# Performance work log

Hardware: AMD Instinct MI355X
Metric: run time of the kernel (lower is better)

## Reference

```python
import jax, jax.numpy as jnp
import numpy as np
import math

B, L, D, K = 4, 2048, 1024, 3
PAD = K // 2
EPS_LN = 1e-5
EPS_NORM = 1e-12


def dwsep_conv(x_bld, dw, dwb, pw, pwb):
    # x_bld: [B, L, D] -> depthwise conv over L (groups=D) then pointwise 1x1
    x = jnp.transpose(x_bld, (0, 2, 1))  # [B, D, L]
    y = jax.lax.conv_general_dilated(
        x, dw, window_strides=(1,), padding=[(PAD, PAD)],
        feature_group_count=D, dimension_numbers=("NCH", "OIH", "NCH"))
    y = y + dwb[None, :, None]
    y = jnp.einsum("bcl,oc->bol", y, pw) + pwb[None, :, None]
    return jnp.transpose(y, (0, 2, 1))  # [B, L, D]


def l2norm(x):
    n = jnp.sqrt(jnp.sum(x * x, axis=-1, keepdims=True))
    return x / jnp.maximum(n, EPS_NORM)


def layernorm(x, g, b):
    mu = jnp.mean(x, axis=-1, keepdims=True)
    var = jnp.mean((x - mu) ** 2, axis=-1, keepdims=True)
    return (x - mu) * jax.lax.rsqrt(var + EPS_LN) * g + b


def setup_inputs() -> dict:
    key = jax.random.key(0)
    ks = jax.random.split(key, 24)
    s = 0.02
    def w(k, shape, scale=s):
        return (jax.random.normal(k, shape, dtype=jnp.float32) * scale)
    inp = {
        "x": jax.random.normal(ks[0], (B, L, D), dtype=jnp.float32),
        "wq": w(ks[1], (D, D)), "bq": jnp.zeros((D,), jnp.float32),
        "wk": w(ks[2], (D, D)), "bk": jnp.zeros((D,), jnp.float32),
        "wv": w(ks[3], (D, D)), "bv": jnp.zeros((D,), jnp.float32),
        "dwq": w(ks[4], (D, 1, K), 0.1), "dwq_b": jnp.zeros((D,), jnp.float32),
        "pwq": w(ks[5], (D, D)), "pwq_b": jnp.zeros((D,), jnp.float32),
        "dwk": w(ks[6], (D, 1, K), 0.1), "dwk_b": jnp.zeros((D,), jnp.float32),
        "pwk": w(ks[7], (D, D)), "pwk_b": jnp.zeros((D,), jnp.float32),
        "dwv": w(ks[8], (D, 1, K), 0.1), "dwv_b": jnp.zeros((D,), jnp.float32),
        "pwv": w(ks[9], (D, D)), "pwv_b": jnp.zeros((D,), jnp.float32),
        "wg": w(ks[10], (D, D)), "bg": jnp.zeros((D,), jnp.float32),
        "wo": w(ks[11], (D, D)), "bo": jnp.zeros((D,), jnp.float32),
        "mem_w": w(ks[12], (D, D)),
        "ln_g": jnp.ones((D,), jnp.float32),
        "ln_b": jnp.zeros((D,), jnp.float32),
    }
    return inp


def reference(x, wq, bq, wk, bk, wv, bv,
              dwq, dwq_b, pwq, pwq_b,
              dwk, dwk_b, pwk, pwk_b,
              dwv, dwv_b, pwv, pwv_b,
              wg, bg, wo, bo, mem_w, ln_g, ln_b):
    residual = x
    Q = jax.nn.silu(jnp.einsum("bld,ed->ble", x, wq) + bq)
    Kt = jax.nn.silu(jnp.einsum("bld,ed->ble", x, wk) + bk)
    V = jax.nn.silu(jnp.einsum("bld,ed->ble", x, wv) + bv)
    Q = dwsep_conv(Q, dwq, dwq_b, pwq, pwq_b)
    Kt = dwsep_conv(Kt, dwk, dwk_b, pwk, pwk_b)
    V = dwsep_conv(V, dwv, dwv_b, pwv, pwv_b)
    Qn = l2norm(Q)
    Kn = l2norm(Kt)
    scores = jnp.einsum("bqd,bkd->bqk", Qn, Kn) / math.sqrt(D)
    attn = jax.nn.softmax(scores, axis=-1)
    attn_out = jnp.einsum("bqk,bkd->bqd", attn, V)
    gate = jax.nn.sigmoid(jnp.einsum("bld,ed->ble", attn_out, wg) + bg)
    gated = gate * attn_out
    out = jnp.einsum("bld,ed->ble", gated, wo) + bo + residual
    out = layernorm(out, ln_g, ln_b)
    mem_pred = jnp.einsum("bld,de->ble", Kn, mem_w)
    mem_loss = jnp.mean((mem_pred - V) ** 2)
    return (out, mem_loss)
```

## Files before the change

### kernel.cpp

```cpp
#include <hip/hip_runtime.h>
#include <stdint.h>

typedef __attribute__((ext_vector_type(8))) short short8;
typedef __attribute__((ext_vector_type(4))) short short4v;
typedef __attribute__((ext_vector_type(4))) float f32x4;

#define DEV static __device__ __forceinline__

static constexpr int LL = 2048;
static constexpr int DD = 1024;
static constexpr long long BLD = 8388608LL;
static constexpr long long SLD = 2097152LL;
static constexpr long long SLLB = 4194304LL;

DEV short f2bf(float f) {
    uint32_t u = __builtin_bit_cast(uint32_t, f);
    u += 0x7fffu + ((u >> 16) & 1u);
    return (short)(u >> 16);
}
DEV float bf2f(short s) {
    uint32_t u = ((uint32_t)(uint16_t)s) << 16;
    return __builtin_bit_cast(float, u);
}

DEV float waveSum(float v) {
#pragma unroll
    for (int o = 32; o; o >>= 1) v += __shfl_down(v, o);
    return v;
}

DEV void gload16(const void* g, void* l) {
    __builtin_amdgcn_global_load_lds(
        (const __attribute__((address_space(1))) uint32_t*)(uintptr_t)g,
        (__attribute__((address_space(3))) uint32_t*)(uintptr_t)l,
        16, 0, 0);
}


__global__ __launch_bounds__(256) void k_zero1(float* p) {
    if (threadIdx.x == 0) *p = 0.f;
}

__global__ __launch_bounds__(256) void k_f32_to_bf16(const float* __restrict__ in,
                                                     short* __restrict__ out, int n8) {
    int i = blockIdx.x * 256 + threadIdx.x;
    if (i >= n8) return;
    const float4* p = (const float4*)(in + (long long)i * 8);
    float4 a = p[0], b = p[1];
    short8 o;
    o[0] = f2bf(a.x); o[1] = f2bf(a.y); o[2] = f2bf(a.z); o[3] = f2bf(a.w);
    o[4] = f2bf(b.x); o[5] = f2bf(b.y); o[6] = f2bf(b.z); o[7] = f2bf(b.w);
    *(short8*)(out + (long long)i * 8) = o;
}

__global__ __launch_bounds__(256) void k_wcat(
    const float* wq, const float* wk, const float* wv,
    const float* pq, const float* pk, const float* pv,
    const float* wg, const float* wo,
    short* Wqkv, short* Pqkv, short* Wg, short* Wo) {
    const int bid = blockIdx.x;
    const int w = bid >> 9;
    const long long i = (long long)((bid & 511) * 256 + threadIdx.x) * 8;
    const float* src; short* dst;
    switch (w) {
        case 0: src = wq; dst = Wqkv;                break;
        case 1: src = wk; dst = Wqkv + 1048576;      break;
        case 2: src = wv; dst = Wqkv + 2097152;      break;
        case 3: src = pq; dst = Pqkv;                break;
        case 4: src = pk; dst = Pqkv + 1048576;      break;
        case 5: src = pv; dst = Pqkv + 2097152;      break;
        case 6: src = wg; dst = Wg;                  break;
        default: src = wo; dst = Wo;                 break;
    }
    const float4* p = (const float4*)(src + i);
    float4 a = p[0], b = p[1];
    short8 o;
    o[0] = f2bf(a.x); o[1] = f2bf(a.y); o[2] = f2bf(a.z); o[3] = f2bf(a.w);
    o[4] = f2bf(b.x); o[5] = f2bf(b.y); o[6] = f2bf(b.z); o[7] = f2bf(b.w);
    *(short8*)(dst + i) = o;
}

__global__ __launch_bounds__(256) void k_biascat(
    const float* bq, const float* bk, const float* bv,
    const float* pq, const float* pk, const float* pv,
    float* bqkv, float* bpw) {
    const int idx = blockIdx.x * 256 + threadIdx.x;
    const int sel = idx >> 10, j = idx & 1023;
    const float* s;
    switch (sel) {
        case 0: s = bq; break; case 1: s = bk; break; case 2: s = bv; break;
        case 3: s = pq; break; case 4: s = pk; break; default: s = pv; break;
    }
    float v = s[j];
    if (sel < 3) bqkv[sel * 1024 + j] = v;
    else         bpw[(sel - 3) * 1024 + j] = v;
}

__global__ __launch_bounds__(256) void k_dwconv3b(const short* __restrict__ in,
                                                  const float* __restrict__ dwq,
                                                  const float* __restrict__ dwk,
                                                  const float* __restrict__ dwv,
                                                  const float* __restrict__ dbq,
                                                  const float* __restrict__ dbk,
                                                  const float* __restrict__ dbv,
                                                  short* __restrict__ outp) {
    const int idx = blockIdx.x * 256 + threadIdx.x;
    const int d8 = idx & 127;
    const int lc = (idx >> 7) & 255;
    const int b  = (idx >> 15) & 3;
    const int br = idx >> 17;
    const float* dw = (br == 0) ? dwq : (br == 1) ? dwk : dwv;
    const float* db = (br == 0) ? dbq : (br == 1) ? dbk : dbv;

    float w[24], bb[8];
    {
        const float4* wp = (const float4*)(dw + d8 * 24);
#pragma unroll
        for (int i = 0; i < 6; i++) {
            float4 t = wp[i];
            w[i * 4 + 0] = t.x; w[i * 4 + 1] = t.y;
            w[i * 4 + 2] = t.z; w[i * 4 + 3] = t.w;
        }
        const float4* bp = (const float4*)(db + d8 * 8);
        float4 t0 = bp[0], t1 = bp[1];
        bb[0] = t0.x; bb[1] = t0.y; bb[2] = t0.z; bb[3] = t0.w;
        bb[4] = t1.x; bb[5] = t1.y; bb[6] = t1.z; bb[7] = t1.w;
    }

    const int l0 = lc * 8;
    const long long base = ((long long)(b * LL + l0)) * 3072 + br * 1024 + d8 * 8;
    short8 xr[10];
#pragma unroll
    for (int i = 0; i < 10; i++) {
        const int l = l0 - 1 + i;
        if (l >= 0 && l < LL) xr[i] = *(const short8*)(in + base + (long long)(i - 1) * 3072);
        else { short8 z = {0, 0, 0, 0, 0, 0, 0, 0}; xr[i] = z; }
    }
#pragma unroll
    for (int j = 0; j < 8; j++) {
        short8 o;
#pragma unroll
        for (int c = 0; c < 8; c++) {
            float v = bb[c] + w[c * 3 + 0] * bf2f(xr[j][c])
                            + w[c * 3 + 1] * bf2f(xr[j + 1][c])
                            + w[c * 3 + 2] * bf2f(xr[j + 2][c]);
            o[c] = f2bf(v);
        }
        *(short8*)(outp + base + (long long)j * 3072) = o;
    }
}

__global__ __launch_bounds__(256) void k_l2norm(short* __restrict__ xp) {
    __shared__ float red[4];
    const long long row = blockIdx.x;
    short* p = xp + row * DD;
    const int t = threadIdx.x;
    short4v v = *(short4v*)(p + t * 4);
    float f0 = bf2f(v[0]), f1 = bf2f(v[1]), f2 = bf2f(v[2]), f3 = bf2f(v[3]);
    float ss = f0 * f0 + f1 * f1 + f2 * f2 + f3 * f3;
    ss = waveSum(ss);
    if ((t & 63) == 0) red[t >> 6] = ss;
    __syncthreads();
    ss = (red[0] + red[1]) + (red[2] + red[3]);
    float s = 1.f / fmaxf(sqrtf(ss), 1e-12f);
    v[0] = f2bf(f0 * s); v[1] = f2bf(f1 * s); v[2] = f2bf(f2 * s); v[3] = f2bf(f3 * s);
    *(short4v*)(p + t * 4) = v;
}

__global__ __launch_bounds__(256) void k_rowsuminv(const short* __restrict__ sp,
                                                   float* __restrict__ rinv) {
    __shared__ float red[4];
    const long long row = blockIdx.x;
    const short* p = sp + row * 2048;
    const int t = threadIdx.x;
    short8 v = *(short8*)(p + t * 8);
    float s = 0.f;
#pragma unroll
    for (int j = 0; j < 8; j++) s += bf2f(v[j]);
    s = waveSum(s);
    if ((t & 63) == 0) red[t >> 6] = s;
    __syncthreads();
    s = (red[0] + red[1]) + (red[2] + red[3]);
    if (t == 0) rinv[row] = 1.f / s;
}

__global__ __launch_bounds__(256) void k_layernorm(float* __restrict__ y,
                                                   const float* __restrict__ g,
                                                   const float* __restrict__ b) {
    __shared__ float redS[4], redQ[4];
    const long long row = blockIdx.x;
    float* p = y + row * DD;
    const int t = threadIdx.x;
    float4 v = *(float4*)(p + t * 4);
    float s = v.x + v.y + v.z + v.w;
    float q = v.x * v.x + v.y * v.y + v.z * v.z + v.w * v.w;
    s = waveSum(s); q = waveSum(q);
    if ((t & 63) == 0) { redS[t >> 6] = s; redQ[t >> 6] = q; }
    __syncthreads();
    s = (redS[0] + redS[1]) + (redS[2] + redS[3]);
    q = (redQ[0] + redQ[1]) + (redQ[2] + redQ[3]);
    float mu = s * (1.f / DD);
    float var = q * (1.f / DD) - mu * mu;
    float rs = rsqrtf(var + 1e-5f);
    float4 o;
    o.x = (v.x - mu) * rs * g[t * 4 + 0] + b[t * 4 + 0];
    o.y = (v.y - mu) * rs * g[t * 4 + 1] + b[t * 4 + 1];
    o.z = (v.z - mu) * rs * g[t * 4 + 2] + b[t * 4 + 2];
    o.w = (v.w - mu) * rs * g[t * 4 + 3] + b[t * 4 + 3];
    *(float4*)(p + t * 4) = o;
}

__global__ __launch_bounds__(256) void k_transpose_bf16(const short* __restrict__ in,
                                                        short* __restrict__ out,
                                                        int rows, int cols) {
    __shared__ short tile[64][65];
    const long long boff = (long long)blockIdx.z * rows * cols;
    in += boff; out += boff;
    const int r0 = blockIdx.y * 64, c0 = blockIdx.x * 64;
    const int t = threadIdx.x;
#pragma unroll
    for (int i = 0; i < 16; i++) {
        int lin = i * 256 + t; int lr = lin >> 6, lc = lin & 63;
        tile[lr][lc] = in[(long long)(r0 + lr) * cols + (c0 + lc)];
    }
    __syncthreads();
#pragma unroll
    for (int i = 0; i < 16; i++) {
        int lin = i * 256 + t; int orr = lin >> 6, oc = lin & 63;
        out[(long long)(c0 + orr) * rows + (r0 + oc)] = tile[oc][orr];
    }
}

__global__ __launch_bounds__(256) void k_transpose_f32_bf16(const float* __restrict__ in,
                                                            short* __restrict__ out,
                                                            int rows, int cols) {
    __shared__ float tile[64][65];
    const int r0 = blockIdx.y * 64, c0 = blockIdx.x * 64;
    const int t = threadIdx.x;
#pragma unroll
    for (int i = 0; i < 16; i++) {
        int lin = i * 256 + t; int lr = lin >> 6, lc = lin & 63;
        tile[lr][lc] = in[(long long)(r0 + lr) * cols + (c0 + lc)];
    }
    __syncthreads();
#pragma unroll
    for (int i = 0; i < 16; i++) {
        int lin = i * 256 + t; int orr = lin >> 6, oc = lin & 63;
        out[(long long)(c0 + orr) * rows + (r0 + oc)] = f2bf(tile[oc][orr]);
    }
}

enum { EPI_SILU, EPI_BIAS, EPI_EXPS, EPI_GATE, EPI_RESID };

template <int EPI>
__global__ __launch_bounds__(256, 4) void gemm(
    const short* __restrict__ A, int lda, long long sAb,
    const short* __restrict__ W, int ldw, long long sWb,
    void* __restrict__ outv, int ldo, long long sOb,
    const float* __restrict__ bias, long long sBias,
    const void* __restrict__ aux,
    int K, float scale) {
    __shared__ short lds[16384];

    const int z = blockIdx.z;
    A += (long long)z * sAb;
    W += (long long)z * sWb;

    const int tid = threadIdx.x;
    const int wid = tid >> 6, lane = tid & 63;
    const int row0 = blockIdx.y * 128, col0 = blockIdx.x * 128;
    const int wrM = (wid >> 1) * 64, wcN = (wid & 1) * 64;
    const int rl = lane & 15, kcl = lane >> 4;

    f32x4 acc[4][4] = {};

    const int srow = tid >> 3;
    const int cswz = (tid & 7) ^ (srow & 7);
    long long offA[4], offB[4];
#pragma unroll
    for (int j = 0; j < 4; j++) {
        const int rr = j * 32 + srow;
        offA[j] = (long long)(row0 + rr) * lda + cswz * 8;
        offB[j] = (long long)(col0 + rr) * ldw + cswz * 8;
    }

    const int nk = K >> 6;
    const int swz0 = (kcl ^ (rl & 7)) * 8;
    const int swz1 = ((kcl + 4) ^ (rl & 7)) * 8;

    for (int t = 0; t < nk; ++t) {
        const short* a = A + (long long)t * 64;
        const short* w = W + (long long)t * 64;
#pragma unroll
        for (int j = 0; j < 4; j++)
            gload16(a + offA[j], lds + (j * 256 + tid) * 8);
#pragma unroll
        for (int j = 0; j < 4; j++)
            gload16(w + offB[j], lds + 8192 + (j * 256 + tid) * 8);
        asm volatile("s_waitcnt vmcnt(0)" ::: "memory");
        __builtin_amdgcn_s_barrier();

        short8 af[4], bfr[4];
#pragma unroll
        for (int mi = 0; mi < 4; mi++)
            af[mi] = *(const short8*)&lds[(wrM + mi * 16 + rl) * 64 + swz0];
#pragma unroll
        for (int ni = 0; ni < 4; ni++)
            bfr[ni] = *(const short8*)&lds[8192 + (wcN + ni * 16 + rl) * 64 + swz0];
        __builtin_amdgcn_s_setprio(1);
#pragma unroll
        for (int mi = 0; mi < 4; mi++)
#pragma unroll
            for (int ni = 0; ni < 4; ni++)
                acc[mi][ni] = __builtin_amdgcn_mfma_f32_16x16x32_bf16(
                    af[mi], bfr[ni], acc[mi][ni], 0, 0, 0);
        __builtin_amdgcn_s_setprio(0);
#pragma unroll
        for (int mi = 0; mi < 4; mi++)
            af[mi] = *(const short8*)&lds[(wrM + mi * 16 + rl) * 64 + swz1];
#pragma unroll
        for (int ni = 0; ni < 4; ni++)
            bfr[ni] = *(const short8*)&lds[8192 + (wcN + ni * 16 + rl) * 64 + swz1];
        __builtin_amdgcn_s_setprio(1);
#pragma unroll
        for (int mi = 0; mi < 4; mi++)
#pragma unroll
            for (int ni = 0; ni < 4; ni++)
                acc[mi][ni] = __builtin_amdgcn_mfma_f32_16x16x32_bf16(
                    af[mi], bfr[ni], acc[mi][ni], 0, 0, 0);
        __builtin_amdgcn_s_setprio(0);
        __builtin_amdgcn_s_barrier();
    }

    const int lr4 = (lane >> 4) * 4;
    float bcol[4];
    if constexpr (EPI == EPI_SILU || EPI == EPI_BIAS || EPI == EPI_GATE || EPI == EPI_RESID) {
        const float* bz = bias + (long long)z * sBias;
#pragma unroll
        for (int ni = 0; ni < 4; ni++) bcol[ni] = bz[col0 + wcN + ni * 16 + rl];
    }
#pragma unroll
    for (int mi = 0; mi < 4; mi++) {
#pragma unroll
        for (int ni = 0; ni < 4; ni++) {
            const int gc = col0 + wcN + ni * 16 + rl;
#pragma unroll
            for (int r = 0; r < 4; r++) {
                const int gr = row0 + wrM + mi * 16 + lr4 + r;
                const long long oi = (long long)gr * ldo + gc;
                float v = acc[mi][ni][r];
                if constexpr (EPI == EPI_SILU) {
                    v += bcol[ni];
                    v = v / (1.f + __expf(-v));
                    ((short*)outv + (long long)z * sOb)[oi] = f2bf(v);
                } else if constexpr (EPI == EPI_BIAS) {
                    ((short*)outv + (long long)z * sOb)[oi] = f2bf(v + bcol[ni]);
                } else if constexpr (EPI == EPI_EXPS) {
                    ((short*)outv + (long long)z * sOb)[oi] = f2bf(__expf(v * scale));
                } else if constexpr (EPI == EPI_GATE) {
                    float g = 1.f / (1.f + __expf(-(v + bcol[ni])));
                    float a = bf2f(((const short*)aux)[oi]);
                    ((short*)outv)[oi] = f2bf(g * a);
                } else if constexpr (EPI == EPI_RESID) {
                    ((float*)outv)[oi] = v + bcol[ni] + ((const float*)aux)[oi];
                }
            }
        }
    }
}

__global__ __launch_bounds__(256, 4) void k_avml(
    const short* __restrict__ P, const short* __restrict__ VT,
    const float* __restrict__ rinv, short* __restrict__ aob,
    const short* __restrict__ kb, const short* __restrict__ MwT,
    const short* __restrict__ vb, float* __restrict__ lossOut) {
    __shared__ short lds[16384];

    const int bid = blockIdx.x;
    const bool isAV = bid < 512;
    const short* A; const short* W;
    int lda, ldw, K, row0, col0;
    const float* rp = nullptr;
    short* outp = nullptr;
    if (isAV) {
        const int z = bid >> 7, rem = bid & 127;
        row0 = (rem >> 3) * 128; col0 = (rem & 7) * 128;
        A = P + (long long)z * SLLB;  lda = 2048;
        W = VT + (long long)z * SLD;  ldw = 2048;
        K = 2048;
        outp = aob + (long long)z * SLD;
        rp = rinv + z * 2048;
    } else {
        const int rem = bid - 512;
        row0 = (rem >> 3) * 128; col0 = (rem & 7) * 128;
        A = kb; lda = 1024; W = MwT; ldw = 1024; K = 1024;
    }

    const int tid = threadIdx.x;
    const int wid = tid >> 6, lane = tid & 63;
    const int wrM = (wid >> 1) * 64, wcN = (wid & 1) * 64;
    const int rl = lane & 15, kcl = lane >> 4;

    f32x4 acc[4][4] = {};

    const int srow = tid >> 3;
    const int cswz = (tid & 7) ^ (srow & 7);
    long long offA[4], offB[4];
#pragma unroll
    for (int j = 0; j < 4; j++) {
        const int rr = j * 32 + srow;
        offA[j] = (long long)(row0 + rr) * lda + cswz * 8;
        offB[j] = (long long)(col0 + rr) * ldw + cswz * 8;
    }

    const int nk = K >> 6;
    const int swz0 = (kcl ^ (rl & 7)) * 8;
    const int swz1 = ((kcl + 4) ^ (rl & 7)) * 8;

    for (int t = 0; t < nk; ++t) {
        const short* a = A + (long long)t * 64;
        const short* w = W + (long long)t * 64;
#pragma unroll
        for (int j = 0; j < 4; j++)
            gload16(a + offA[j], lds + (j * 256 + tid) * 8);
#pragma unroll
        for (int j = 0; j < 4; j++)
            gload16(w + offB[j], lds + 8192 + (j * 256 + tid) * 8);
        asm volatile("s_waitcnt vmcnt(0)" ::: "memory");
        __builtin_amdgcn_s_barrier();

        short8 af[4], bfr[4];
#pragma unroll
        for (int mi = 0; mi < 4; mi++)
            af[mi] = *(const short8*)&lds[(wrM + mi * 16 + rl) * 64 + swz0];
#pragma unroll
        for (int ni = 0; ni < 4; ni++)
            bfr[ni] = *(const short8*)&lds[8192 + (wcN + ni * 16 + rl) * 64 + swz0];
        __builtin_amdgcn_s_setprio(1);
#pragma unroll
        for (int mi = 0; mi < 4; mi++)
#pragma unroll
            for (int ni = 0; ni < 4; ni++)
                acc[mi][ni] = __builtin_amdgcn_mfma_f32_16x16x32_bf16(
                    af[mi], bfr[ni], acc[mi][ni], 0, 0, 0);
        __builtin_amdgcn_s_setprio(0);
#pragma unroll
        for (int mi = 0; mi < 4; mi++)
            af[mi] = *(const short8*)&lds[(wrM + mi * 16 + rl) * 64 + swz1];
#pragma unroll
        for (int ni = 0; ni < 4; ni++)
            bfr[ni] = *(const short8*)&lds[8192 + (wcN + ni * 16 + rl) * 64 + swz1];
        __builtin_amdgcn_s_setprio(1);
#pragma unroll
        for (int mi = 0; mi < 4; mi++)
#pragma unroll
            for (int ni = 0; ni < 4; ni++)
                acc[mi][ni] = __builtin_amdgcn_mfma_f32_16x16x32_bf16(
                    af[mi], bfr[ni], acc[mi][ni], 0, 0, 0);
        __builtin_amdgcn_s_setprio(0);
        __builtin_amdgcn_s_barrier();
    }

    const int lr4 = (lane >> 4) * 4;
    if (isAV) {
#pragma unroll
        for (int mi = 0; mi < 4; mi++) {
#pragma unroll
            for (int ni = 0; ni < 4; ni++) {
                const int gc = col0 + wcN + ni * 16 + rl;
#pragma unroll
                for (int r = 0; r < 4; r++) {
                    const int gr = row0 + wrM + mi * 16 + lr4 + r;
                    outp[(long long)gr * 1024 + gc] = f2bf(acc[mi][ni][r] * rp[gr]);
                }
            }
        }
    } else {
        float lsum = 0.f;
#pragma unroll
        for (int mi = 0; mi < 4; mi++) {
#pragma unroll
            for (int ni = 0; ni < 4; ni++) {
                const int gc = col0 + wcN + ni * 16 + rl;
#pragma unroll
                for (int r = 0; r < 4; r++) {
                    const int gr = row0 + wrM + mi * 16 + lr4 + r;
                    float dd = acc[mi][ni][r] - bf2f(vb[(long long)gr * 1024 + gc]);
                    lsum += dd * dd;
                }
            }
        }
        lsum = waveSum(lsum);
        if (lane == 0) atomicAdd(lossOut, lsum * (1.f / (float)BLD));
    }
}


extern "C" void kernel_launch(void* const* d_in, const int* in_sizes, int n_in,
                              void* d_out, int out_size, void* d_ws, size_t ws_size,
                              hipStream_t stream) {
    const float* x    = (const float*)d_in[0];
    const float* wq   = (const float*)d_in[1];
    const float* bq   = (const float*)d_in[2];
    const float* wk   = (const float*)d_in[3];
    const float* bk   = (const float*)d_in[4];
    const float* wvw  = (const float*)d_in[5];
    const float* bvv  = (const float*)d_in[6];
    const float* dwq  = (const float*)d_in[7];
    const float* dwqb = (const float*)d_in[8];
    const float* pwq  = (const float*)d_in[9];
    const float* pwqb = (const float*)d_in[10];
    const float* dwk  = (const float*)d_in[11];
    const float* dwkb = (const float*)d_in[12];
    const float* pwk  = (const float*)d_in[13];
    const float* pwkb = (const float*)d_in[14];
    const float* dwv  = (const float*)d_in[15];
    const float* dwvb = (const float*)d_in[16];
    const float* pwv  = (const float*)d_in[17];
    const float* pwvb = (const float*)d_in[18];
    const float* wg   = (const float*)d_in[19];
    const float* bg   = (const float*)d_in[20];
    const float* wo   = (const float*)d_in[21];
    const float* bo   = (const float*)d_in[22];
    const float* memw = (const float*)d_in[23];
    const float* lng  = (const float*)d_in[24];
    const float* lnb  = (const float*)d_in[25];

    float* out = (float*)d_out;
    float* loss = out + BLD;

    char* base = (char*)d_ws;
    size_t off = 0;
    auto take = [&](size_t n) -> char* {
        char* p = base + off;
        off += (n + 255) & ~(size_t)255;
        return p;
    };
    const size_t WB = (size_t)DD * DD * 2;
    const size_t XB = (size_t)BLD * 2;
    short* Wqkv = (short*)take(3 * WB);
    short* Pqkv = (short*)take(3 * WB);
    short* Wgb  = (short*)take(WB);
    short* Wob  = (short*)take(WB);
    short* MwT  = (short*)take(WB);
    float* bqkv = (float*)take(3072 * 4);
    float* bpw  = (float*)take(3072 * 4);
    float* rinv = (float*)take(8192 * 4);
    short* xb   = (short*)take(XB);
    short* pre  = (short*)take(3 * XB);
    short* post = (short*)take(3 * XB);

    short* qb = pre;
    short* kb = pre + BLD;
    short* vb = pre + 2 * BLD;
    short* scores = post;
    short* VT = post + 2 * BLD;
    short* aob = xb;
    short* gated = post;
    (void)ws_size; (void)in_sizes; (void)n_in; (void)out_size;

    const long long sLD = SLD;
    const long long sLLb = SLLB;

    k_zero1<<<1, 1, 0, stream>>>(loss);
    k_wcat<<<4096, 256, 0, stream>>>(wq, wk, wvw, pwq, pwk, pwv, wg, wo,
                                     Wqkv, Pqkv, Wgb, Wob);
    k_biascat<<<24, 256, 0, stream>>>(bq, bk, bvv, pwqb, pwkb, pwvb, bqkv, bpw);
    k_transpose_f32_bf16<<<dim3(16, 16, 1), 256, 0, stream>>>(memw, MwT, DD, DD);
    k_f32_to_bf16<<<4096, 256, 0, stream>>>(x, xb, (int)(BLD / 8));

    gemm<EPI_SILU><<<dim3(24, 64, 1), 256, 0, stream>>>(
        xb, 1024, 0, Wqkv, 1024, 0, pre, 3072, 0, bqkv, 0, nullptr, 1024, 0.f);

    k_dwconv3b<<<1536, 256, 0, stream>>>(pre, dwq, dwk, dwv, dwqb, dwkb, dwvb, post);

    gemm<EPI_BIAS><<<dim3(8, 64, 3), 256, 0, stream>>>(
        post, 3072, 1024, Pqkv, 1024, (long long)DD * DD, qb, 1024, BLD,
        bpw, 1024, nullptr, 1024, 0.f);

    k_l2norm<<<16384, 256, 0, stream>>>(qb);
    k_transpose_bf16<<<dim3(16, 32, 4), 256, 0, stream>>>(vb, VT, 2048, 1024);

    gemm<EPI_EXPS><<<dim3(16, 16, 4), 256, 0, stream>>>(
        qb, 1024, sLD, kb, 1024, sLD, scores, 2048, sLLb,
        nullptr, 0, nullptr, 1024, 0.03125f);
    k_rowsuminv<<<8192, 256, 0, stream>>>(scores, rinv);

    k_avml<<<1024, 256, 0, stream>>>(scores, VT, rinv, aob, kb, MwT, vb, loss);

    gemm<EPI_GATE><<<dim3(8, 64, 1), 256, 0, stream>>>(
        aob, 1024, 0, Wgb, 1024, 0, gated, 1024, 0, bg, 0, aob, 1024, 0.f);

    gemm<EPI_RESID><<<dim3(8, 64, 1), 256, 0, stream>>>(
        gated, 1024, 0, Wob, 1024, 0, out, 1024, 0, bo, 0, x, 1024, 0.f);
    k_layernorm<<<8192, 256, 0, stream>>>(out, lng, lnb);
}
```

Measured before the change: 379.9 us.

## Fold L2 norm scaling into score epilogue and merge prep kernels

The in-place L2 normalization of Q and K is replaced by computing per-row inverse norms only. These are applied as row and column scales in the exp-score GEMM epilogue and in the memory-loss epilogue. The V transpose and the norm computation share one launch, and the weight/bias/x conversions, the memw transpose and the loss zeroing merge into one prep kernel. This removes a read-write pass over Q/K and several launches, at the cost of scoring against unnormalized bf16 Q/K values, which changes rounding.

```diff
diff --git a/kernel.cpp b/kernel.cpp
--- a/kernel.cpp
+++ b/kernel.cpp
@@ -36,64 +36,76 @@
         16, 0, 0);
 }
 
-
-__global__ __launch_bounds__(256) void k_zero1(float* p) {
-    if (threadIdx.x == 0) *p = 0.f;
-}
-
-__global__ __launch_bounds__(256) void k_f32_to_bf16(const float* __restrict__ in,
-                                                     short* __restrict__ out, int n8) {
-    int i = blockIdx.x * 256 + threadIdx.x;
-    if (i >= n8) return;
-    const float4* p = (const float4*)(in + (long long)i * 8);
-    float4 a = p[0], b = p[1];
-    short8 o;
-    o[0] = f2bf(a.x); o[1] = f2bf(a.y); o[2] = f2bf(a.z); o[3] = f2bf(a.w);
-    o[4] = f2bf(b.x); o[5] = f2bf(b.y); o[6] = f2bf(b.z); o[7] = f2bf(b.w);
-    *(short8*)(out + (long long)i * 8) = o;
-}
-
-__global__ __launch_bounds__(256) void k_wcat(
+__global__ __launch_bounds__(256) void k_prep(
+    const float* __restrict__ x,
     const float* wq, const float* wk, const float* wv,
     const float* pq, const float* pk, const float* pv,
     const float* wg, const float* wo,
-    short* Wqkv, short* Pqkv, short* Wg, short* Wo) {
+    const float* bq, const float* bk, const float* bv,
+    const float* pqb, const float* pkb, const float* pvb,
+    const float* __restrict__ memw,
+    short* Wqkv, short* Pqkv, short* Wg, short* Wo,
+    float* bqkv, float* bpw, short* MwT, short* xb, float* loss) {
+    __shared__ float tile[64][65];
     const int bid = blockIdx.x;
-    const int w = bid >> 9;
-    const long long i = (long long)((bid & 511) * 256 + threadIdx.x) * 8;
-    const float* src; short* dst;
-    switch (w) {
-        case 0: src = wq; dst = Wqkv;                break;
-        case 1: src = wk; dst = Wqkv + 1048576;      break;
-        case 2: src = wv; dst = Wqkv + 2097152;      break;
-        case 3: src = pq; dst = Pqkv;                break;
-        case 4: src = pk; dst = Pqkv + 1048576;      break;
-        case 5: src = pv; dst = Pqkv + 2097152;      break;
-        case 6: src = wg; dst = Wg;                  break;
-        default: src = wo; dst = Wo;                 break;
-    }
-    const float4* p = (const float4*)(src + i);
-    float4 a = p[0], b = p[1];
-    short8 o;
-    o[0] = f2bf(a.x); o[1] = f2bf(a.y); o[2] = f2bf(a.z); o[3] = f2bf(a.w);
-    o[4] = f2bf(b.x); o[5] = f2bf(b.y); o[6] = f2bf(b.z); o[7] = f2bf(b.w);
-    *(short8*)(dst + i) = o;
-}
-
-__global__ __launch_bounds__(256) void k_biascat(
-    const float* bq, const float* bk, const float* bv,
-    const float* pq, const float* pk, const float* pv,
-    float* bqkv, float* bpw) {
-    const int idx = blockIdx.x * 256 + threadIdx.x;
-    const int sel = idx >> 10, j = idx & 1023;
-    const float* s;
-    switch (sel) {
-        case 0: s = bq; break; case 1: s = bk; break; case 2: s = bv; break;
-        case 3: s = pq; break; case 4: s = pk; break; default: s = pv; break;
-    }
-    float v = s[j];
-    if (sel < 3) bqkv[sel * 1024 + j] = v;
-    else         bpw[(sel - 3) * 1024 + j] = v;
+    const int t = threadIdx.x;
+
+    if (bid < 4096) {
+        const int w = bid >> 9;
+        const long long i = (long long)((bid & 511) * 256 + t) * 8;
+        const float* src; short* dst;
+        switch (w) {
+            case 0: src = wq; dst = Wqkv;                break;
+            case 1: src = wk; dst = Wqkv + 1048576;      break;
+            case 2: src = wv; dst = Wqkv + 2097152;      break;
+            case 3: src = pq; dst = Pqkv;                break;
+            case 4: src = pk; dst = Pqkv + 1048576;      break;
+            case 5: src = pv; dst = Pqkv + 2097152;      break;
+            case 6: src = wg; dst = Wg;                  break;
+            default: src = wo; dst = Wo;                 break;
+        }
+        const float4* p = (const float4*)(src + i);
+        float4 a = p[0], b = p[1];
+        short8 o;
+        o[0] = f2bf(a.x); o[1] = f2bf(a.y); o[2] = f2bf(a.z); o[3] = f2bf(a.w);
+        o[4] = f2bf(b.x); o[5] = f2bf(b.y); o[6] = f2bf(b.z); o[7] = f2bf(b.w);
+        *(short8*)(dst + i) = o;
+    } else if (bid < 4120) {
+        const int idx = (bid - 4096) * 256 + t;
+        const int sel = idx >> 10, j = idx & 1023;
+        const float* s;
+        switch (sel) {
+            case 0: s = bq; break; case 1: s = bk; break; case 2: s = bv; break;
+            case 3: s = pqb; break; case 4: s = pkb; break; default: s = pvb; break;
+        }
+        float v = s[j];
+        if (sel < 3) bqkv[sel * 1024 + j] = v;
+        else         bpw[(sel - 3) * 1024 + j] = v;
+    } else if (bid < 4376) {
+        const int tt = bid - 4120;
+        const int r0 = (tt >> 4) * 64, c0 = (tt & 15) * 64;
+#pragma unroll
+        for (int i = 0; i < 16; i++) {
+            int lin = i * 256 + t; int lr = lin >> 6, lc = lin & 63;
+            tile[lr][lc] = memw[(long long)(r0 + lr) * DD + (c0 + lc)];
+        }
+        __syncthreads();
+#pragma unroll
+        for (int i = 0; i < 16; i++) {
+            int lin = i * 256 + t; int orr = lin >> 6, oc = lin & 63;
+            MwT[(long long)(c0 + orr) * DD + (r0 + oc)] = f2bf(tile[oc][orr]);
+        }
+    } else if (bid < 8472) {
+        const long long i = (long long)((bid - 4376) * 256 + t) * 8;
+        const float4* p = (const float4*)(x + i);
+        float4 a = p[0], b = p[1];
+        short8 o;
+        o[0] = f2bf(a.x); o[1] = f2bf(a.y); o[2] = f2bf(a.z); o[3] = f2bf(a.w);
+        o[4] = f2bf(b.x); o[5] = f2bf(b.y); o[6] = f2bf(b.z); o[7] = f2bf(b.w);
+        *(short8*)(xb + i) = o;
+    } else {
+        if (t == 0) *loss = 0.f;
+    }
 }
 
 __global__ __launch_bounds__(256) void k_dwconv3b(const short* __restrict__ in,
@@ -117,9 +129,9 @@
         const float4* wp = (const float4*)(dw + d8 * 24);
 #pragma unroll
         for (int i = 0; i < 6; i++) {
-            float4 t = wp[i];
-            w[i * 4 + 0] = t.x; w[i * 4 + 1] = t.y;
-            w[i * 4 + 2] = t.z; w[i * 4 + 3] = t.w;
+            float4 tt = wp[i];
+            w[i * 4 + 0] = tt.x; w[i * 4 + 1] = tt.y;
+            w[i * 4 + 2] = tt.z; w[i * 4 + 3] = tt.w;
         }
         const float4* bp = (const float4*)(db + d8 * 8);
         float4 t0 = bp[0], t1 = bp[1];
@@ -150,21 +162,42 @@
     }
 }
 
-__global__ __launch_bounds__(256) void k_l2norm(short* __restrict__ xp) {
+__global__ __launch_bounds__(256) void k_vt_norm(const short* __restrict__ vb,
+                                                 short* __restrict__ VT,
+                                                 const short* __restrict__ qkb,
+                                                 float* __restrict__ ninv) {
+    __shared__ short tile[64][65];
     __shared__ float red[4];
-    const long long row = blockIdx.x;
-    short* p = xp + row * DD;
+    const int bid = blockIdx.x;
     const int t = threadIdx.x;
-    short4v v = *(short4v*)(p + t * 4);
-    float f0 = bf2f(v[0]), f1 = bf2f(v[1]), f2 = bf2f(v[2]), f3 = bf2f(v[3]);
-    float ss = f0 * f0 + f1 * f1 + f2 * f2 + f3 * f3;
-    ss = waveSum(ss);
-    if ((t & 63) == 0) red[t >> 6] = ss;
-    __syncthreads();
-    ss = (red[0] + red[1]) + (red[2] + red[3]);
-    float s = 1.f / fmaxf(sqrtf(ss), 1e-12f);
-    v[0] = f2bf(f0 * s); v[1] = f2bf(f1 * s); v[2] = f2bf(f2 * s); v[3] = f2bf(f3 * s);
-    *(short4v*)(p + t * 4) = v;
+    if (bid < 2048) {
+        const int z = bid >> 9, tt = bid & 511;
+        const int r0 = (tt >> 4) * 64, c0 = (tt & 15) * 64;
+        const short* in = vb + (long long)z * SLD;
+        short* out = VT + (long long)z * SLD;
+#pragma unroll
+        for (int i = 0; i < 16; i++) {
+            int lin = i * 256 + t; int lr = lin >> 6, lc = lin & 63;
+            tile[lr][lc] = in[(long long)(r0 + lr) * 1024 + (c0 + lc)];
+        }
+        __syncthreads();
+#pragma unroll
+        for (int i = 0; i < 16; i++) {
+            int lin = i * 256 + t; int orr = lin >> 6, oc = lin & 63;
+            out[(long long)(c0 + orr) * 2048 + (r0 + oc)] = tile[oc][orr];
+        }
+    } else {
+        const long long row = bid - 2048;
+        const short* p = qkb + row * DD;
+        short4v v = *(const short4v*)(p + t * 4);
+        float f0 = bf2f(v[0]), f1 = bf2f(v[1]), f2 = bf2f(v[2]), f3 = bf2f(v[3]);
+        float ss = f0 * f0 + f1 * f1 + f2 * f2 + f3 * f3;
+        ss = waveSum(ss);
+        if ((t & 63) == 0) red[t >> 6] = ss;
+        __syncthreads();
+        ss = (red[0] + red[1]) + (red[2] + red[3]);
+        if (t == 0) ninv[row] = 1.f / fmaxf(sqrtf(ss), 1e-12f);
+    }
 }
 
 __global__ __launch_bounds__(256) void k_rowsuminv(const short* __restrict__ sp,
@@ -210,46 +243,6 @@
     *(float4*)(p + t * 4) = o;
 }
 
-__global__ __launch_bounds__(256) void k_transpose_bf16(const short* __restrict__ in,
-                                                        short* __restrict__ out,
-                                                        int rows, int cols) {
-    __shared__ short tile[64][65];
-    const long long boff = (long long)blockIdx.z * rows * cols;
-    in += boff; out += boff;
-    const int r0 = blockIdx.y * 64, c0 = blockIdx.x * 64;
-    const int t = threadIdx.x;
-#pragma unroll
-    for (int i = 0; i < 16; i++) {
-        int lin = i * 256 + t; int lr = lin >> 6, lc = lin & 63;
-        tile[lr][lc] = in[(long long)(r0 + lr) * cols + (c0 + lc)];
-    }
-    __syncthreads();
-#pragma unroll
-    for (int i = 0; i < 16; i++) {
-        int lin = i * 256 + t; int orr = lin >> 6, oc = lin & 63;
-        out[(long long)(c0 + orr) * rows + (r0 + oc)] = tile[oc][orr];
-    }
-}
-
-__global__ __launch_bounds__(256) void k_transpose_f32_bf16(const float* __restrict__ in,
-                                                            short* __restrict__ out,
-                                                            int rows, int cols) {
-    __shared__ float tile[64][65];
-    const int r0 = blockIdx.y * 64, c0 = blockIdx.x * 64;
-    const int t = threadIdx.x;
-#pragma unroll
-    for (int i = 0; i < 16; i++) {
-        int lin = i * 256 + t; int lr = lin >> 6, lc = lin & 63;
-        tile[lr][lc] = in[(long long)(r0 + lr) * cols + (c0 + lc)];
-    }
-    __syncthreads();
-#pragma unroll
-    for (int i = 0; i < 16; i++) {
-        int lin = i * 256 + t; int orr = lin >> 6, oc = lin & 63;
-        out[(long long)(c0 + orr) * rows + (r0 + oc)] = f2bf(tile[oc][orr]);
-    }
-}
-
 enum { EPI_SILU, EPI_BIAS, EPI_EXPS, EPI_GATE, EPI_RESID };
 
 template <int EPI>
@@ -339,6 +332,12 @@
 #pragma unroll
         for (int ni = 0; ni < 4; ni++) bcol[ni] = bz[col0 + wcN + ni * 16 + rl];
     }
+    if constexpr (EPI == EPI_EXPS) {
+        const float* kz = (const float*)aux + (long long)z * 2048;
+#pragma unroll
+        for (int ni = 0; ni < 4; ni++) bcol[ni] = kz[col0 + wcN + ni * 16 + rl];
+    }
+    const float* qz = (EPI == EPI_EXPS) ? bias + (long long)z * sBias : nullptr;
 #pragma unroll
     for (int mi = 0; mi < 4; mi++) {
 #pragma unroll
@@ -356,7 +355,8 @@
                 } else if constexpr (EPI == EPI_BIAS) {
                     ((short*)outv + (long long)z * sOb)[oi] = f2bf(v + bcol[ni]);
                 } else if constexpr (EPI == EPI_EXPS) {
-                    ((short*)outv + (long long)z * sOb)[oi] = f2bf(__expf(v * scale));
+                    ((short*)outv + (long long)z * sOb)[oi] =
+                        f2bf(__expf(v * qz[gr] * bcol[ni] * scale));
                 } else if constexpr (EPI == EPI_GATE) {
                     float g = 1.f / (1.f + __expf(-(v + bcol[ni])));
                     float a = bf2f(((const short*)aux)[oi]);
@@ -373,7 +373,8 @@
     const short* __restrict__ P, const short* __restrict__ VT,
     const float* __restrict__ rinv, short* __restrict__ aob,
     const short* __restrict__ kb, const short* __restrict__ MwT,
-    const short* __restrict__ vb, float* __restrict__ lossOut) {
+    const short* __restrict__ vb, const float* __restrict__ kinv,
+    float* __restrict__ lossOut) {
     __shared__ short lds[16384];
 
     const int bid = blockIdx.x;
@@ -485,7 +486,7 @@
 #pragma unroll
                 for (int r = 0; r < 4; r++) {
                     const int gr = row0 + wrM + mi * 16 + lr4 + r;
-                    float dd = acc[mi][ni][r] - bf2f(vb[(long long)gr * 1024 + gc]);
+                    float dd = acc[mi][ni][r] * kinv[gr] - bf2f(vb[(long long)gr * 1024 + gc]);
                     lsum += dd * dd;
                 }
             }
@@ -546,6 +547,7 @@
     float* bqkv = (float*)take(3072 * 4);
     float* bpw  = (float*)take(3072 * 4);
     float* rinv = (float*)take(8192 * 4);
+    float* ninv = (float*)take(16384 * 4);
     short* xb   = (short*)take(XB);
     short* pre  = (short*)take(3 * XB);
     short* post = (short*)take(3 * XB);
@@ -557,17 +559,17 @@
     short* VT = post + 2 * BLD;
     short* aob = xb;
     short* gated = post;
+    float* qinv = ninv;
+    float* kinv = ninv + 8192;
     (void)ws_size; (void)in_sizes; (void)n_in; (void)out_size;
 
     const long long sLD = SLD;
     const long long sLLb = SLLB;
 
-    k_zero1<<<1, 1, 0, stream>>>(loss);
-    k_wcat<<<4096, 256, 0, stream>>>(wq, wk, wvw, pwq, pwk, pwv, wg, wo,
-                                     Wqkv, Pqkv, Wgb, Wob);
-    k_biascat<<<24, 256, 0, stream>>>(bq, bk, bvv, pwqb, pwkb, pwvb, bqkv, bpw);
-    k_transpose_f32_bf16<<<dim3(16, 16, 1), 256, 0, stream>>>(memw, MwT, DD, DD);
-    k_f32_to_bf16<<<4096, 256, 0, stream>>>(x, xb, (int)(BLD / 8));
+    k_prep<<<8473, 256, 0, stream>>>(
+        x, wq, wk, wvw, pwq, pwk, pwv, wg, wo,
+        bq, bk, bvv, pwqb, pwkb, pwvb, memw,
+        Wqkv, Pqkv, Wgb, Wob, bqkv, bpw, MwT, xb, loss);
 
     gemm<EPI_SILU><<<dim3(24, 64, 1), 256, 0, stream>>>(
         xb, 1024, 0, Wqkv, 1024, 0, pre, 3072, 0, bqkv, 0, nullptr, 1024, 0.f);
@@ -578,15 +580,14 @@
         post, 3072, 1024, Pqkv, 1024, (long long)DD * DD, qb, 1024, BLD,
         bpw, 1024, nullptr, 1024, 0.f);
 
-    k_l2norm<<<16384, 256, 0, stream>>>(qb);
-    k_transpose_bf16<<<dim3(16, 32, 4), 256, 0, stream>>>(vb, VT, 2048, 1024);
+    k_vt_norm<<<18432, 256, 0, stream>>>(vb, VT, qb, ninv);
 
     gemm<EPI_EXPS><<<dim3(16, 16, 4), 256, 0, stream>>>(
         qb, 1024, sLD, kb, 1024, sLD, scores, 2048, sLLb,
-        nullptr, 0, nullptr, 1024, 0.03125f);
+        qinv, 2048, kinv, 1024, 0.03125f);
     k_rowsuminv<<<8192, 256, 0, stream>>>(scores, rinv);
 
-    k_avml<<<1024, 256, 0, stream>>>(scores, VT, rinv, aob, kb, MwT, vb, loss);
+    k_avml<<<1024, 256, 0, stream>>>(scores, VT, rinv, aob, kb, MwT, vb, kinv, loss);
 
     gemm<EPI_GATE><<<dim3(8, 64, 1), 256, 0, stream>>>(
         aob, 1024, 0, Wgb, 1024, 0, gated, 1024, 0, bg, 0, aob, 1024, 0.f);
```

After: 379.0 us. About the same (-0.2%).
